# Kernel optimization log

Measured on AMD Instinct MI355X. Metric: run time of the kernel, lower is better.

The kernel has to match this reference:

```python
import jax, jax.numpy as jnp
import numpy as np

ALPHA = 1000.0  # softmin temperature from the original module


def setup_inputs() -> dict:
    key = jax.random.key(0)
    ks = jax.random.split(key, 10)
    B, D, H, E, K = 8192, 784, 256, 32, 512
    s = 0.05  # small init scale to keep activations/distances numerically sane
    return {
        "x": jax.random.normal(ks[0], (B, D), jnp.float32),
        "cluster_reps": jax.random.normal(ks[1], (K, E), jnp.float32),
        "W1": jax.random.normal(ks[2], (D, H), jnp.float32) * s,
        "b1": jnp.zeros((H,), jnp.float32),
        "W2": jax.random.normal(ks[3], (H, E), jnp.float32) * s,
        "b2": jnp.zeros((E,), jnp.float32),
        "W3": jax.random.normal(ks[4], (E, H), jnp.float32) * s,
        "b3": jnp.zeros((H,), jnp.float32),
        "W4": jax.random.normal(ks[5], (H, D), jnp.float32) * s,
        "b4": jnp.zeros((D,), jnp.float32),
    }


def reference(x, cluster_reps, W1, b1, W2, b2, W3, b3, W4, b4):
    # --- autoencoder: 2-layer MLP encoder / decoder ---
    h = jax.nn.relu(x @ W1 + b1)            # [B, H]
    embeddings = h @ W2 + b2                # [B, E]
    h2 = jax.nn.relu(embeddings @ W3 + b3)  # [B, H]
    reconstruction = h2 @ W4 + b4           # [B, D]

    # --- squared distances to cluster reps: [B, K] ---
    diff = embeddings[:, None, :] - cluster_reps[None, :, :]  # [B, K, E]
    distances = jnp.sum(diff * diff, axis=2)                  # [B, K]

    # --- stable softmin-weighted distances ---
    min_dist = jnp.min(distances, axis=1, keepdims=True)       # [B, 1]
    exponentials = jnp.exp(-ALPHA * (distances - min_dist))    # [B, K]
    sum_exponentials = jnp.sum(exponentials, axis=1, keepdims=True)
    weighted_dists = distances * (exponentials / sum_exponentials)

    return (weighted_dists, distances, reconstruction, embeddings)
```

## Files before the change

### kernel.cpp

```cpp
#include <hip/hip_runtime.h>
#include <cstddef>

#define NB 8192
#define ND 784
#define NH 256
#define NE 32
#define NK 512
#define ALPHA_F 1000.0f

typedef _Float16 h8 __attribute__((ext_vector_type(8)));
typedef float f32x4 __attribute__((ext_vector_type(4)));

#define TW1 25
#define TN1 8
#define NBW1 200
#define TW4 8
#define TN4 25
#define NBW4 200
#define NBW2 8
#define NBW3 8

__global__ __launch_bounds__(256)
void prep4_kernel(const float* __restrict__ W1, _Float16* __restrict__ w1thi,
                  _Float16* __restrict__ w1tlo,
                  const float* __restrict__ W4, _Float16* __restrict__ w4thi,
                  _Float16* __restrict__ w4tlo,
                  const float* __restrict__ W2, _Float16* __restrict__ w2thi,
                  _Float16* __restrict__ w2tlo,
                  const float* __restrict__ W3, _Float16* __restrict__ w3thi,
                  _Float16* __restrict__ w3tlo) {
    __shared__ float tile[32][33];
    const int b   = blockIdx.x;
    const int tid = threadIdx.x;

    const float* W; _Float16 *hi, *lo; int K, N, kt, nt;
    if (b < NBW1) {
        W = W1; hi = w1thi; lo = w1tlo; K = ND; N = NH;
        kt = b % TW1; nt = b / TW1;
    } else if (b < NBW1 + NBW4) {
        const int bb = b - NBW1;
        W = W4; hi = w4thi; lo = w4tlo; K = NH; N = ND;
        kt = bb % TW4; nt = bb / TW4;
    } else if (b < NBW1 + NBW4 + NBW2) {
        W = W2; hi = w2thi; lo = w2tlo; K = NH; N = NE;
        kt = b - (NBW1 + NBW4); nt = 0;
    } else {
        W = W3; hi = w3thi; lo = w3tlo; K = NE; N = NH;
        kt = 0; nt = b - (NBW1 + NBW4 + NBW2);
    }
    const int k0 = kt * 32, n0 = nt * 32;
    const int row = tid >> 3, c4 = (tid & 7) * 4;
    #pragma unroll
    for (int j = 0; j < 4; ++j) {
        const int k = k0 + row, n = n0 + c4 + j;
        tile[row][c4 + j] = (k < K && n < N) ? W[(size_t)k * N + n] : 0.f;
    }
    __syncthreads();
    const int n = n0 + row;
    if (n < N) {
        #pragma unroll
        for (int j = 0; j < 4; ++j) {
            const int k = k0 + c4 + j;
            if (k < K) {
                float w = tile[c4 + j][row];
                _Float16 hh = (_Float16)w;
                float r = w - (float)hh;
                hi[(size_t)n * K + k] = hh;
                lo[(size_t)n * K + k] = (_Float16)(r * 2048.0f);
            }
        }
    }
}

__global__ __launch_bounds__(512, 1)
void mega_kernel(const float* __restrict__ x, const float* __restrict__ reps,
                 const _Float16* __restrict__ w1thi, const _Float16* __restrict__ w1tlo,
                 const _Float16* __restrict__ w2thi, const _Float16* __restrict__ w2tlo,
                 const _Float16* __restrict__ w3thi, const _Float16* __restrict__ w3tlo,
                 const _Float16* __restrict__ w4thi, const _Float16* __restrict__ w4tlo,
                 const float* __restrict__ b1, const float* __restrict__ b2,
                 const float* __restrict__ b3, const float* __restrict__ b4,
                 float* __restrict__ emb_g, float* __restrict__ recon_g,
                 float* __restrict__ dist_g, float* __restrict__ wout_g) {
    __shared__ __align__(16) unsigned char lds[135936];
    _Float16* R0h  = (_Float16*)lds;
    _Float16* sA   = (_Float16*)(lds + 81920);
    _Float16* hP   = (_Float16*)(lds + 92160);
    float*    es   = (float*)(lds + 125952);
    _Float16* eP   = (_Float16*)(lds + 130560);
    float*    rmin = (float*)(lds + 135680);
    float*    rinv = (float*)(lds + 135808);

    const int tid  = threadIdx.x;
    const int lane = tid & 63;
    const int wv   = tid >> 6;
    const int li   = lane & 15;
    const int kq   = (lane >> 4) * 8;
    const int quad = lane >> 4;
    const int r0   = blockIdx.x * 32;

    const float c1 = 1.0f / 2048.0f;
    const float c2 = c1 * c1;

    {
        _Float16* sBhi = R0h;
        _Float16* sBlo = R0h + 2 * 256 * 40;
        _Float16* sAhi = sA;
        _Float16* sAlo = sA + 2 * 32 * 40;
        const int arow = (tid & 127) >> 2;
        const int ak   = (tid & 3) * 8;
        const int brow = tid >> 1;
        const int bk   = (tid & 1) * 16;
        const float*    pA  = x + (size_t)(r0 + arow) * ND;
        const _Float16* pBh = w1thi + (size_t)brow * ND;
        const _Float16* pBl = w1tlo + (size_t)brow * ND;

        float araw[8];
        h8 rb0, rb1, rb2, rb3;

        auto pf = [&](int s) {
            if (tid < 128) {
                const int k = s * 32 + ak;
                if (k + 8 <= ND) {
                    f32x4 v0 = *(const f32x4*)(pA + k);
                    f32x4 v1 = *(const f32x4*)(pA + k + 4);
                    #pragma unroll
                    for (int j = 0; j < 4; ++j) {
                        araw[j] = v0[j]; araw[4 + j] = v1[j];
                    }
                } else {
                    #pragma unroll
                    for (int j = 0; j < 8; ++j) araw[j] = 0.f;
                }
            }
            const int kb = s * 32 + bk;
            rb0 = (kb + 8  <= ND) ? *(const h8*)(pBh + kb)     : (h8){};
            rb1 = (kb + 16 <= ND) ? *(const h8*)(pBh + kb + 8) : (h8){};
            rb2 = (kb + 8  <= ND) ? *(const h8*)(pBl + kb)     : (h8){};
            rb3 = (kb + 16 <= ND) ? *(const h8*)(pBl + kb + 8) : (h8){};
        };
        auto cm = [&](int buf) {
            if (tid < 128) {
                h8 hi, lo;
                #pragma unroll
                for (int j = 0; j < 8; ++j) {
                    float v = araw[j];
                    _Float16 hh = (_Float16)v;
                    hi[j] = hh;
                    lo[j] = (_Float16)((v - (float)hh) * 2048.0f);
                }
                *(h8*)&sAhi[buf * 32 * 40 + arow * 40 + ak] = hi;
                *(h8*)&sAlo[buf * 32 * 40 + arow * 40 + ak] = lo;
            }
            *(h8*)&sBhi[buf * 256 * 40 + brow * 40 + bk]     = rb0;
            *(h8*)&sBhi[buf * 256 * 40 + brow * 40 + bk + 8] = rb1;
            *(h8*)&sBlo[buf * 256 * 40 + brow * 40 + bk]     = rb2;
            *(h8*)&sBlo[buf * 256 * 40 + brow * 40 + bk + 8] = rb3;
        };

        pf(0); cm(0); pf(1);
        __syncthreads();

        f32x4 a0[2][2] = {}, a1[2][2] = {}, a2[2][2] = {};
        for (int s = 0; s < 25; ++s) {
            const int buf = s & 1;
            h8 fah[2], fal[2], fbh[2], fbl[2];
            #pragma unroll
            for (int mt = 0; mt < 2; ++mt) {
                const int ao = buf * 32 * 40 + (mt * 16 + li) * 40 + kq;
                fah[mt] = *(const h8*)&sAhi[ao];
                fal[mt] = *(const h8*)&sAlo[ao];
            }
            #pragma unroll
            for (int nt = 0; nt < 2; ++nt) {
                const int bo = buf * 256 * 40 + (wv * 32 + nt * 16 + li) * 40 + kq;
                fbh[nt] = *(const h8*)&sBhi[bo];
                fbl[nt] = *(const h8*)&sBlo[bo];
            }
            #pragma unroll
            for (int mt = 0; mt < 2; ++mt)
                #pragma unroll
                for (int nt = 0; nt < 2; ++nt) {
                    a0[mt][nt] = __builtin_amdgcn_mfma_f32_16x16x32_f16(
                        fah[mt], fbh[nt], a0[mt][nt], 0, 0, 0);
                    a1[mt][nt] = __builtin_amdgcn_mfma_f32_16x16x32_f16(
                        fah[mt], fbl[nt], a1[mt][nt], 0, 0, 0);
                    a1[mt][nt] = __builtin_amdgcn_mfma_f32_16x16x32_f16(
                        fal[mt], fbh[nt], a1[mt][nt], 0, 0, 0);
                    a2[mt][nt] = __builtin_amdgcn_mfma_f32_16x16x32_f16(
                        fal[mt], fbl[nt], a2[mt][nt], 0, 0, 0);
                }
            if (s + 1 < 25) { cm((s + 1) & 1); if (s + 2 < 25) pf(s + 2); }
            __syncthreads();
        }
        _Float16* hhi = hP;
        _Float16* hlo = hP + 32 * 264;
        #pragma unroll
        for (int nt = 0; nt < 2; ++nt) {
            const int n = wv * 32 + nt * 16 + li;
            const float bv = b1[n];
            #pragma unroll
            for (int mt = 0; mt < 2; ++mt)
                #pragma unroll
                for (int r = 0; r < 4; ++r) {
                    const int m = mt * 16 + quad * 4 + r;
                    float v = a0[mt][nt][r] + c1 * a1[mt][nt][r]
                            + c2 * a2[mt][nt][r] + bv;
                    v = fmaxf(v, 0.f);
                    _Float16 hh = (_Float16)v;
                    hhi[m * 264 + n] = hh;
                    hlo[m * 264 + n] = (_Float16)((v - (float)hh) * 2048.0f);
                }
        }
    }
    __syncthreads();

    {
        _Float16* w2h = R0h;
        _Float16* w2l = R0h + 32 * 264;
        #pragma unroll
        for (int i = 0; i < 2; ++i) {
            const int cc  = tid + i * 512;
            const int row = cc >> 5, off = (cc & 31) * 8;
            *(h8*)&w2h[row * 264 + off] = *(const h8*)(w2thi + row * 256 + off);
            *(h8*)&w2l[row * 264 + off] = *(const h8*)(w2tlo + row * 256 + off);
        }
    }
    __syncthreads();
    if (wv < 4) {
        const int mt = wv >> 1, nt = wv & 1;
        _Float16* hhi = hP;
        _Float16* hlo = hP + 32 * 264;
        _Float16* w2h = R0h;
        _Float16* w2l = R0h + 32 * 264;
        f32x4 e0 = {}, e1 = {}, e2 = {};
        #pragma unroll
        for (int ks = 0; ks < 8; ++ks) {
            h8 ah = *(const h8*)&hhi[(mt * 16 + li) * 264 + ks * 32 + kq];
            h8 al = *(const h8*)&hlo[(mt * 16 + li) * 264 + ks * 32 + kq];
            h8 bh = *(const h8*)&w2h[(nt * 16 + li) * 264 + ks * 32 + kq];
            h8 bl = *(const h8*)&w2l[(nt * 16 + li) * 264 + ks * 32 + kq];
            e0 = __builtin_amdgcn_mfma_f32_16x16x32_f16(ah, bh, e0, 0, 0, 0);
            e1 = __builtin_amdgcn_mfma_f32_16x16x32_f16(ah, bl, e1, 0, 0, 0);
            e1 = __builtin_amdgcn_mfma_f32_16x16x32_f16(al, bh, e1, 0, 0, 0);
            e2 = __builtin_amdgcn_mfma_f32_16x16x32_f16(al, bl, e2, 0, 0, 0);
        }
        const int ccol = nt * 16 + li;
        const float bv = b2[ccol];
        _Float16* ehi = eP;
        _Float16* elo = eP + 32 * 40;
        #pragma unroll
        for (int r = 0; r < 4; ++r) {
            const int m = mt * 16 + quad * 4 + r;
            float v = e0[r] + c1 * e1[r] + c2 * e2[r] + bv;
            es[m * 36 + ccol] = v;
            _Float16 hh = (_Float16)v;
            ehi[m * 40 + ccol] = hh;
            elo[m * 40 + ccol] = (_Float16)((v - (float)hh) * 2048.0f);
            emb_g[(size_t)(r0 + m) * NE + ccol] = v;
        }
    }
    __syncthreads();

    {
        _Float16* w3h = R0h;
        _Float16* w3l = R0h + 256 * 40;
        #pragma unroll
        for (int i = 0; i < 2; ++i) {
            const int cc  = tid + i * 512;
            const int row = cc >> 2, off = (cc & 3) * 8;
            *(h8*)&w3h[row * 40 + off] = *(const h8*)(w3thi + row * 32 + off);
            *(h8*)&w3l[row * 40 + off] = *(const h8*)(w3tlo + row * 32 + off);
        }
    }
    __syncthreads();
    {
        const int n0 = wv * 32;
        _Float16* w3h  = R0h;
        _Float16* w3l  = R0h + 256 * 40;
        _Float16* ehi  = eP;
        _Float16* elo  = eP + 32 * 40;
        _Float16* h2hi = hP;
        _Float16* h2lo = hP + 32 * 264;
        h8 ah[2], al[2];
        #pragma unroll
        for (int mt = 0; mt < 2; ++mt) {
            ah[mt] = *(const h8*)&ehi[(mt * 16 + li) * 40 + kq];
            al[mt] = *(const h8*)&elo[(mt * 16 + li) * 40 + kq];
        }
        #pragma unroll
        for (int nt = 0; nt < 2; ++nt) {
            h8 bh = *(const h8*)&w3h[(n0 + nt * 16 + li) * 40 + kq];
            h8 bl = *(const h8*)&w3l[(n0 + nt * 16 + li) * 40 + kq];
            const int col = n0 + nt * 16 + li;
            const float bv = b3[col];
            #pragma unroll
            for (int mt = 0; mt < 2; ++mt) {
                f32x4 q0 = {}, q1 = {}, q2 = {};
                q0 = __builtin_amdgcn_mfma_f32_16x16x32_f16(ah[mt], bh, q0, 0, 0, 0);
                q1 = __builtin_amdgcn_mfma_f32_16x16x32_f16(ah[mt], bl, q1, 0, 0, 0);
                q1 = __builtin_amdgcn_mfma_f32_16x16x32_f16(al[mt], bh, q1, 0, 0, 0);
                q2 = __builtin_amdgcn_mfma_f32_16x16x32_f16(al[mt], bl, q2, 0, 0, 0);
                #pragma unroll
                for (int r = 0; r < 4; ++r) {
                    const int m = mt * 16 + quad * 4 + r;
                    float v = q0[r] + c1 * q1[r] + c2 * q2[r] + bv;
                    v = fmaxf(v, 0.f);
                    _Float16 hh = (_Float16)v;
                    h2hi[m * 264 + col] = hh;
                    h2lo[m * 264 + col] = (_Float16)((v - (float)hh) * 2048.0f);
                }
            }
        }
    }
    __syncthreads();

    {
        _Float16* sBhi = R0h;
        _Float16* sBlo = R0h + 2 * 128 * 40;
        _Float16* h2hi = hP;
        _Float16* h2lo = hP + 32 * 264;
        const int brow = tid >> 2;
        const int bk4  = (tid & 3) * 8;
        h8 rbh, rbl;
        auto pf = [&](int ss) {
            int rg = (ss >> 3) * 128 + brow;
            if (rg > ND - 1) rg = ND - 1;
            const int k = (ss & 7) * 32 + bk4;
            rbh = *(const h8*)(w4thi + (size_t)rg * NH + k);
            rbl = *(const h8*)(w4tlo + (size_t)rg * NH + k);
        };
        auto cm = [&](int ss) {
            const int buf = ss & 1;
            *(h8*)&sBhi[buf * 128 * 40 + brow * 40 + bk4] = rbh;
            *(h8*)&sBlo[buf * 128 * 40 + brow * 40 + bk4] = rbl;
        };
        pf(0); cm(0); pf(1);
        __syncthreads();

        f32x4 q0[2] = {}, q1[2] = {};
        for (int ss = 0; ss < 56; ++ss) {
            const int buf = ss & 1, ks = ss & 7;
            h8 fbh = *(const h8*)&sBhi[buf * 128 * 40 + (wv * 16 + li) * 40 + kq];
            h8 fbl = *(const h8*)&sBlo[buf * 128 * 40 + (wv * 16 + li) * 40 + kq];
            #pragma unroll
            for (int mt = 0; mt < 2; ++mt) {
                h8 ah = *(const h8*)&h2hi[(mt * 16 + li) * 264 + ks * 32 + kq];
                h8 al = *(const h8*)&h2lo[(mt * 16 + li) * 264 + ks * 32 + kq];
                q0[mt] = __builtin_amdgcn_mfma_f32_16x16x32_f16(ah, fbh, q0[mt], 0, 0, 0);
                q1[mt] = __builtin_amdgcn_mfma_f32_16x16x32_f16(ah, fbl, q1[mt], 0, 0, 0);
                q1[mt] = __builtin_amdgcn_mfma_f32_16x16x32_f16(al, fbh, q1[mt], 0, 0, 0);
            }
            if (ss + 1 < 56) { cm(ss + 1); if (ss + 2 < 56) pf(ss + 2); }
            __syncthreads();
            if (ks == 7) {
                const int n = (ss >> 3) * 128 + wv * 16 + li;
                if (n < ND) {
                    const float bv = b4[n];
                    #pragma unroll
                    for (int mt = 0; mt < 2; ++mt)
                        #pragma unroll
                        for (int r = 0; r < 4; ++r) {
                            const int m = mt * 16 + quad * 4 + r;
                            recon_g[(size_t)(r0 + m) * ND + n] =
                                q0[mt][r] + c1 * q1[mt][r] + bv;
                        }
                }
                #pragma unroll
                for (int mt = 0; mt < 2; ++mt) { q0[mt] = {}; q1[mt] = {}; }
            }
        }
    }
    __syncthreads();

    {
        float* tr = (float*)R0h;
        const float* rp = reps + (size_t)tid * NE;
        f32x4 rv[8];
        #pragma unroll
        for (int e4 = 0; e4 < 8; ++e4) rv[e4] = ((const f32x4*)rp)[e4];

        float d[32];
        #pragma unroll
        for (int r = 0; r < 32; ++r) {
            float a = 0.f;
            #pragma unroll
            for (int e4 = 0; e4 < 8; ++e4) {
                f32x4 ev = *(const f32x4*)&es[r * 36 + e4 * 4];
                #pragma unroll
                for (int j = 0; j < 4; ++j) {
                    float t = ev[j] - rv[e4][j];
                    a = fmaf(t, t, a);
                }
            }
            d[r] = a;
            tr[r * 520 + tid] = a;
        }
        __syncthreads();
        #pragma unroll
        for (int p = 0; p < 4; ++p) {
            const int rr = wv * 4 + p;
            f32x4 a = *(const f32x4*)&tr[rr * 520 + lane * 8];
            f32x4 b = *(const f32x4*)&tr[rr * 520 + lane * 8 + 4];
            float m = fminf(fminf(fminf(a[0], a[1]), fminf(a[2], a[3])),
                            fminf(fminf(b[0], b[1]), fminf(b[2], b[3])));
            #pragma unroll
            for (int off = 32; off > 0; off >>= 1)
                m = fminf(m, __shfl_xor(m, off, 64));
            if (lane == 0) rmin[rr] = m;
        }
        __syncthreads();
        float e[32];
        #pragma unroll
        for (int r = 0; r < 32; ++r) {
            e[r] = expf(-ALPHA_F * (d[r] - rmin[r]));
            tr[r * 520 + tid] = e[r];
        }
        __syncthreads();
        #pragma unroll
        for (int p = 0; p < 4; ++p) {
            const int rr = wv * 4 + p;
            f32x4 a = *(const f32x4*)&tr[rr * 520 + lane * 8];
            f32x4 b = *(const f32x4*)&tr[rr * 520 + lane * 8 + 4];
            float s = ((a[0] + a[1]) + (a[2] + a[3])) +
                      ((b[0] + b[1]) + (b[2] + b[3]));
            #pragma unroll
            for (int off = 32; off > 0; off >>= 1)
                s += __shfl_xor(s, off, 64);
            if (lane == 0) rinv[rr] = 1.0f / s;
        }
        __syncthreads();
        #pragma unroll
        for (int r = 0; r < 32; ++r) {
            const size_t row = (size_t)(r0 + r);
            dist_g[row * NK + tid] = d[r];
            wout_g[row * NK + tid] = d[r] * (e[r] * rinv[r]);
        }
    }
}

__global__ __launch_bounds__(256)
void splitw2_kernel(const float* __restrict__ W1, _Float16* __restrict__ w1thi,
                    _Float16* __restrict__ w1tlo,
                    const float* __restrict__ W4, _Float16* __restrict__ w4thi,
                    _Float16* __restrict__ w4tlo) {
    const int b = blockIdx.x;
    const float* W; _Float16 *hi, *lo; int K, N, n;
    if (b < NH) { W = W1; hi = w1thi; lo = w1tlo; K = ND; N = NH; n = b; }
    else        { W = W4; hi = w4thi; lo = w4tlo; K = NH; N = ND; n = b - NH; }
    for (int k = threadIdx.x; k < K; k += 256) {
        float w = W[(size_t)k * N + n];
        _Float16 hh = (_Float16)w;
        float r = w - (float)hh;
        hi[(size_t)n * K + k] = hh;
        lo[(size_t)n * K + k] = (_Float16)(r * 2048.0f);
    }
}

template<int TERMS, bool RELU, bool SPLITA, int MT>
__global__ __launch_bounds__(256)
void mfma_gemm3(const float* __restrict__ Af32,
                const _Float16* __restrict__ Ahi_g,
                const _Float16* __restrict__ Alo_g,
                const _Float16* __restrict__ WThi,
                const _Float16* __restrict__ WTlo,
                const float* __restrict__ bias, float* __restrict__ C,
                int N, int K, int KS) {
    constexpr int BM  = MT * 32;
    constexpr int ACH = BM / 64;
    constexpr int AS  = BM * 40;
    constexpr int BS  = 64 * 40;
    __shared__ __align__(16) _Float16 smem[2 * BM * 40 * 2 + 2 * 64 * 40 * 2];
    _Float16* sAhi = smem;
    _Float16* sAlo = sAhi + 2 * BM * 40;
    _Float16* sBhi = sAlo + 2 * BM * 40;
    _Float16* sBlo = sBhi + 2 * 64 * 40;

    const int tid = threadIdx.x;
    const int bm  = blockIdx.x * BM;
    const int bn  = blockIdx.y * 64;

    const int arow = (ACH == 1) ? (tid >> 2) : (tid >> 1);
    const int ak   = (ACH == 1) ? ((tid & 3) * 8) : ((tid & 1) * 16);
    const int brow = tid >> 2;
    const int bk   = (tid & 3) * 8;

    const float*    pA32 = SPLITA ? Af32 + (size_t)(bm + arow) * K : nullptr;
    const _Float16* pAhi = SPLITA ? nullptr : Ahi_g + (size_t)(bm + arow) * K;
    const _Float16* pAlo = SPLITA ? nullptr : Alo_g + (size_t)(bm + arow) * K;
    int brow_g = bn + brow; if (brow_g > N - 1) brow_g = N - 1;
    const _Float16* pBhi = WThi + (size_t)brow_g * K;
    const _Float16* pBlo = WTlo + (size_t)brow_g * K;

    float araw[ACH * 8];
    h8 rahi[ACH], ralo[ACH];
    h8 rbhi, rblo;

    auto prefetch = [&](int s) {
        #pragma unroll
        for (int c = 0; c < ACH; ++c) {
            const int k = s * 32 + ak + c * 8;
            if (SPLITA) {
                if (k + 8 <= K) {
                    f32x4 v0 = *(const f32x4*)(pA32 + k);
                    f32x4 v1 = *(const f32x4*)(pA32 + k + 4);
                    #pragma unroll
                    for (int j = 0; j < 4; ++j) {
                        araw[c * 8 + j]     = v0[j];
                        araw[c * 8 + 4 + j] = v1[j];
                    }
                } else {
                    #pragma unroll
                    for (int j = 0; j < 8; ++j) araw[c * 8 + j] = 0.f;
                }
            } else {
                rahi[c] = (k + 8 <= K) ? *(const h8*)(pAhi + k) : (h8){};
                ralo[c] = (k + 8 <= K) ? *(const h8*)(pAlo + k) : (h8){};
            }
        }
        const int kb = s * 32 + bk;
        rbhi = (kb + 8 <= K) ? *(const h8*)(pBhi + kb) : (h8){};
        rblo = (kb + 8 <= K) ? *(const h8*)(pBlo + kb) : (h8){};
    };

    auto commit = [&](int buf) {
        #pragma unroll
        for (int c = 0; c < ACH; ++c) {
            h8 hi, lo;
            if (SPLITA) {
                #pragma unroll
                for (int j = 0; j < 8; ++j) {
                    float v = araw[c * 8 + j];
                    _Float16 hh = (_Float16)v;
                    hi[j] = hh;
                    lo[j] = (_Float16)((v - (float)hh) * 2048.0f);
                }
            } else { hi = rahi[c]; lo = ralo[c]; }
            *(h8*)&sAhi[buf * AS + arow * 40 + ak + c * 8] = hi;
            *(h8*)&sAlo[buf * AS + arow * 40 + ak + c * 8] = lo;
        }
        *(h8*)&sBhi[buf * BS + brow * 40 + bk] = rbhi;
        *(h8*)&sBlo[buf * BS + brow * 40 + bk] = rblo;
    };

    prefetch(0);
    commit(0);
    prefetch(1);
    __syncthreads();

    const int lane = tid & 63;
    const int wv   = tid >> 6;
    const int wm   = (wv >> 1) * (MT * 16);
    const int wn   = (wv & 1) * 32;
    const int li   = lane & 15;
    const int kq   = (lane >> 4) * 8;

    f32x4 acc0[MT][2] = {};
    f32x4 acc1[MT][2] = {};
    f32x4 acc2[MT][2] = {};

    for (int s = 0; s < KS; ++s) {
        const int buf = s & 1;
        h8 fahi[MT], falo[MT], fbhi[2], fblo[2];
        #pragma unroll
        for (int mt = 0; mt < MT; ++mt) {
            const int ao = buf * AS + (wm + mt * 16 + li) * 40 + kq;
            fahi[mt] = *(const h8*)&sAhi[ao];
            falo[mt] = *(const h8*)&sAlo[ao];
        }
        #pragma unroll
        for (int nt = 0; nt < 2; ++nt) {
            const int bo = buf * BS + (wn + nt * 16 + li) * 40 + kq;
            fbhi[nt] = *(const h8*)&sBhi[bo];
            fblo[nt] = *(const h8*)&sBlo[bo];
        }
        #pragma unroll
        for (int mt = 0; mt < MT; ++mt)
            #pragma unroll
            for (int nt = 0; nt < 2; ++nt) {
                acc0[mt][nt] = __builtin_amdgcn_mfma_f32_16x16x32_f16(
                    fahi[mt], fbhi[nt], acc0[mt][nt], 0, 0, 0);
                acc1[mt][nt] = __builtin_amdgcn_mfma_f32_16x16x32_f16(
                    fahi[mt], fblo[nt], acc1[mt][nt], 0, 0, 0);
                acc1[mt][nt] = __builtin_amdgcn_mfma_f32_16x16x32_f16(
                    falo[mt], fbhi[nt], acc1[mt][nt], 0, 0, 0);
                if (TERMS == 4)
                    acc2[mt][nt] = __builtin_amdgcn_mfma_f32_16x16x32_f16(
                        falo[mt], fblo[nt], acc2[mt][nt], 0, 0, 0);
            }
        if (s + 1 < KS) {
            commit((s + 1) & 1);
            if (s + 2 < KS) prefetch(s + 2);
        }
        __syncthreads();
    }

    const float c1 = 1.0f / 2048.0f;
    const float c2 = c1 * c1;
    const int quad = lane >> 4;
    #pragma unroll
    for (int nt = 0; nt < 2; ++nt) {
        const int n = bn + wn + nt * 16 + li;
        if (n < N) {
            const float bv = bias[n];
            #pragma unroll
            for (int mt = 0; mt < MT; ++mt) {
                #pragma unroll
                for (int r = 0; r < 4; ++r) {
                    const int m = bm + wm + mt * 16 + quad * 4 + r;
                    float v = acc0[mt][nt][r] + c1 * acc1[mt][nt][r];
                    if (TERMS == 4) v += c2 * acc2[mt][nt][r];
                    v += bv;
                    if (RELU) v = fmaxf(v, 0.f);
                    C[(size_t)m * N + n] = v;
                }
            }
        }
    }
}

__global__ __launch_bounds__(256)
void mid_kernel(const float* __restrict__ h, const float* __restrict__ W2,
                const float* __restrict__ b2, const float* __restrict__ W3,
                const float* __restrict__ b3, float* __restrict__ emb,
                _Float16* __restrict__ h2hi, _Float16* __restrict__ h2lo) {
    __shared__ float es[16][32];
    const int tid = threadIdx.x;
    const int r0  = blockIdx.x * 16;

    #pragma unroll
    for (int half = 0; half < 2; ++half) {
        const int o   = tid + half * 256;
        const int row = o >> 5;
        const int col = o & 31;
        const float* hrow = h + (size_t)(r0 + row) * NH;
        float acc0 = 0.f, acc1 = 0.f;
        #pragma unroll 4
        for (int k = 0; k < NH; k += 4) {
            float4 hv = *(const float4*)(hrow + k);
            acc0 = fmaf(hv.x, W2[(k + 0) * NE + col], acc0);
            acc1 = fmaf(hv.y, W2[(k + 1) * NE + col], acc1);
            acc0 = fmaf(hv.z, W2[(k + 2) * NE + col], acc0);
            acc1 = fmaf(hv.w, W2[(k + 3) * NE + col], acc1);
        }
        float v = acc0 + acc1 + b2[col];
        es[row][col] = v;
        emb[(size_t)r0 * NE + o] = v;
    }
    __syncthreads();

    const int col = tid;
    float acc[16];
    #pragma unroll
    for (int r = 0; r < 16; ++r) acc[r] = 0.f;
    #pragma unroll
    for (int k = 0; k < NE; ++k) {
        float w = W3[k * NH + col];
        #pragma unroll
        for (int r = 0; r < 16; ++r) acc[r] = fmaf(es[r][k], w, acc[r]);
    }
    const float bb = b3[col];
    #pragma unroll
    for (int r = 0; r < 16; ++r) {
        float v = acc[r] + bb;
        v = v > 0.f ? v : 0.f;
        _Float16 hh = (_Float16)v;
        float rr = v - (float)hh;
        h2hi[(size_t)(r0 + r) * NH + col] = hh;
        h2lo[(size_t)(r0 + r) * NH + col] = (_Float16)(rr * 2048.0f);
    }
}

__global__ __launch_bounds__(512, 4)
void dist_kernel(const float* __restrict__ emb, const float* __restrict__ reps,
                 float* __restrict__ dist, float* __restrict__ wout) {
    __shared__ float es[8][32];
    __shared__ float tr[8][520];
    __shared__ float rmin[8];
    __shared__ float rinv[8];

    const int tid = threadIdx.x;
    const int r0  = blockIdx.x * 8;

    if (tid < 256) es[tid >> 5][tid & 31] = emb[(size_t)r0 * NE + tid];

    const float* rp = reps + (size_t)tid * NE;
    f32x4 rv[8];
    #pragma unroll
    for (int e4 = 0; e4 < 8; ++e4) rv[e4] = ((const f32x4*)rp)[e4];
    __syncthreads();

    float d[8];
    #pragma unroll
    for (int r = 0; r < 8; ++r) {
        float a = 0.f;
        #pragma unroll
        for (int e4 = 0; e4 < 8; ++e4) {
            f32x4 ev = *(const f32x4*)&es[r][e4 * 4];
            #pragma unroll
            for (int j = 0; j < 4; ++j) {
                float t = ev[j] - rv[e4][j];
                a = fmaf(t, t, a);
            }
        }
        d[r] = a;
    }

    const int lane = tid & 63;
    const int wv   = tid >> 6;

    #pragma unroll
    for (int r = 0; r < 8; ++r) tr[r][tid] = d[r];
    __syncthreads();
    {
        f32x4 a = *(const f32x4*)&tr[wv][lane * 8];
        f32x4 b = *(const f32x4*)&tr[wv][lane * 8 + 4];
        float m = fminf(fminf(fminf(a[0], a[1]), fminf(a[2], a[3])),
                        fminf(fminf(b[0], b[1]), fminf(b[2], b[3])));
        #pragma unroll
        for (int off = 32; off > 0; off >>= 1)
            m = fminf(m, __shfl_xor(m, off, 64));
        if (lane == 0) rmin[wv] = m;
    }
    __syncthreads();

    float e[8];
    #pragma unroll
    for (int r = 0; r < 8; ++r) {
        e[r] = expf(-ALPHA_F * (d[r] - rmin[r]));
        tr[r][tid] = e[r];
    }
    __syncthreads();
    {
        f32x4 a = *(const f32x4*)&tr[wv][lane * 8];
        f32x4 b = *(const f32x4*)&tr[wv][lane * 8 + 4];
        float s = ((a[0] + a[1]) + (a[2] + a[3])) +
                  ((b[0] + b[1]) + (b[2] + b[3]));
        #pragma unroll
        for (int off = 32; off > 0; off >>= 1)
            s += __shfl_xor(s, off, 64);
        if (lane == 0) rinv[wv] = 1.0f / s;
    }
    __syncthreads();

    #pragma unroll
    for (int r = 0; r < 8; ++r) {
        const size_t row = (size_t)(r0 + r);
        dist[row * NK + tid] = d[r];
        wout[row * NK + tid] = d[r] * (e[r] * rinv[r]);
    }
}

extern "C" void kernel_launch(void* const* d_in, const int* in_sizes, int n_in,
                              void* d_out, int out_size, void* d_ws, size_t ws_size,
                              hipStream_t stream) {
    const float* x    = (const float*)d_in[0];
    const float* reps = (const float*)d_in[1];
    const float* W1   = (const float*)d_in[2];
    const float* b1   = (const float*)d_in[3];
    const float* W2   = (const float*)d_in[4];
    const float* b2   = (const float*)d_in[5];
    const float* W3   = (const float*)d_in[6];
    const float* b3   = (const float*)d_in[7];
    const float* W4   = (const float*)d_in[8];
    const float* b4   = (const float*)d_in[9];

    float* out   = (float*)d_out;
    float* wout  = out;
    float* dist  = out + (size_t)NB * NK;
    float* recon = out + (size_t)2 * NB * NK;
    float* emb   = out + (size_t)2 * NB * NK + (size_t)NB * ND;

    const size_t nW14 = (size_t)ND * NH;
    const size_t nW23 = (size_t)NE * NH;
    const size_t wneed = (4 * nW14 + 4 * nW23) * sizeof(_Float16);

    if (d_ws != nullptr && ws_size >= wneed) {
        _Float16* w1thi = (_Float16*)d_ws;
        _Float16* w1tlo = w1thi + nW14;
        _Float16* w4thi = w1tlo + nW14;
        _Float16* w4tlo = w4thi + nW14;
        _Float16* w2thi = w4tlo + nW14;
        _Float16* w2tlo = w2thi + nW23;
        _Float16* w3thi = w2tlo + nW23;
        _Float16* w3tlo = w3thi + nW23;

        prep4_kernel<<<NBW1 + NBW4 + NBW2 + NBW3, 256, 0, stream>>>(
            W1, w1thi, w1tlo, W4, w4thi, w4tlo,
            W2, w2thi, w2tlo, W3, w3thi, w3tlo);

        mega_kernel<<<NB / 32, 512, 0, stream>>>(
            x, reps, w1thi, w1tlo, w2thi, w2tlo, w3thi, w3tlo, w4thi, w4tlo,
            b1, b2, b3, b4, emb, recon, dist, wout);
    } else {
        float* h = dist;
        _Float16* h2hi  = (_Float16*)(dist + (size_t)NB * NH);
        _Float16* h2lo  = h2hi + (size_t)NB * NH;
        _Float16* w1thi = (_Float16*)wout;
        _Float16* w1tlo = w1thi + (size_t)NH * ND;
        _Float16* w4thi = w1tlo + (size_t)NH * ND;
        _Float16* w4tlo = w4thi + (size_t)ND * NH;

        splitw2_kernel<<<NH + ND, 256, 0, stream>>>(W1, w1thi, w1tlo,
                                                    W4, w4thi, w4tlo);
        mfma_gemm3<4, true, true, 2><<<dim3(128, 4), 256, 0, stream>>>(
            x, nullptr, nullptr, w1thi, w1tlo, b1, h, NH, ND, 25);
        mid_kernel<<<NB / 16, 256, 0, stream>>>(h, W2, b2, W3, b3,
                                                emb, h2hi, h2lo);
        mfma_gemm3<3, false, false, 4><<<dim3(64, 13), 256, 0, stream>>>(
            nullptr, h2hi, h2lo, w4thi, w4tlo, b4, recon, ND, NH, 8);
        dist_kernel<<<NB / 8, 512, 0, stream>>>(emb, reps, dist, wout);
    }
}
```

Measured before the change: 166.1 us.

## Double mega_kernel block to 1024 threads and split per-wave tiles across 16 waves

The fused kernel now launches 1024 threads (16 waves) per 32-row block instead of 512. The GEMM1, GEMM3 and GEMM4 stages are retiled so each wave owns one 16-wide N tile (or one M/N tile pair). The distance/softmin stage splits the 32 rows into two 16-row halves, each with its own LDS scratch, and recomputes exp at write-out instead of holding it in registers. The aim is more latency hiding per CU, given that the large LDS footprint allows only one block per CU. In exchange, each wave reuses less data from each LDS fragment load and the register budget per thread is tighter, so spills are possible.

```diff
diff --git a/kernel.cpp b/kernel.cpp
--- a/kernel.cpp
+++ b/kernel.cpp
@@ -72,7 +72,9 @@
     }
 }
 
-__global__ __launch_bounds__(512, 1)
+#define HSTR 264
+
+__global__ __launch_bounds__(1024, 4)
 void mega_kernel(const float* __restrict__ x, const float* __restrict__ reps,
                  const _Float16* __restrict__ w1thi, const _Float16* __restrict__ w1tlo,
                  const _Float16* __restrict__ w2thi, const _Float16* __restrict__ w2tlo,
@@ -87,7 +89,8 @@
     _Float16* sA   = (_Float16*)(lds + 81920);
     _Float16* hP   = (_Float16*)(lds + 92160);
     float*    es   = (float*)(lds + 125952);
-    _Float16* eP   = (_Float16*)(lds + 130560);
+    _Float16* eh   = (_Float16*)(lds + 130560);
+    _Float16* el   = (_Float16*)(lds + 133120);
     float*    rmin = (float*)(lds + 135680);
     float*    rinv = (float*)(lds + 135808);
 
@@ -107,16 +110,18 @@
         _Float16* sBlo = R0h + 2 * 256 * 40;
         _Float16* sAhi = sA;
         _Float16* sAlo = sA + 2 * 32 * 40;
-        const int arow = (tid & 127) >> 2;
+        const int arow = (tid & 255) >> 3;
+        const int aro  = tid >> 2;
         const int ak   = (tid & 3) * 8;
-        const int brow = tid >> 1;
-        const int bk   = (tid & 1) * 16;
-        const float*    pA  = x + (size_t)(r0 + arow) * ND;
+        const int brow = tid >> 2;
+        const int bk   = (tid & 3) * 8;
+        (void)arow;
+        const float*    pA  = x + (size_t)(r0 + aro) * ND;
         const _Float16* pBh = w1thi + (size_t)brow * ND;
         const _Float16* pBl = w1tlo + (size_t)brow * ND;
 
         float araw[8];
-        h8 rb0, rb1, rb2, rb3;
+        h8 rbh, rbl;
 
         auto pf = [&](int s) {
             if (tid < 128) {
@@ -134,10 +139,8 @@
                 }
             }
             const int kb = s * 32 + bk;
-            rb0 = (kb + 8  <= ND) ? *(const h8*)(pBh + kb)     : (h8){};
-            rb1 = (kb + 16 <= ND) ? *(const h8*)(pBh + kb + 8) : (h8){};
-            rb2 = (kb + 8  <= ND) ? *(const h8*)(pBl + kb)     : (h8){};
-            rb3 = (kb + 16 <= ND) ? *(const h8*)(pBl + kb + 8) : (h8){};
+            rbh = (kb + 8 <= ND) ? *(const h8*)(pBh + kb) : (h8){};
+            rbl = (kb + 8 <= ND) ? *(const h8*)(pBl + kb) : (h8){};
         };
         auto cm = [&](int buf) {
             if (tid < 128) {
@@ -149,115 +152,95 @@
                     hi[j] = hh;
                     lo[j] = (_Float16)((v - (float)hh) * 2048.0f);
                 }
-                *(h8*)&sAhi[buf * 32 * 40 + arow * 40 + ak] = hi;
-                *(h8*)&sAlo[buf * 32 * 40 + arow * 40 + ak] = lo;
-            }
-            *(h8*)&sBhi[buf * 256 * 40 + brow * 40 + bk]     = rb0;
-            *(h8*)&sBhi[buf * 256 * 40 + brow * 40 + bk + 8] = rb1;
-            *(h8*)&sBlo[buf * 256 * 40 + brow * 40 + bk]     = rb2;
-            *(h8*)&sBlo[buf * 256 * 40 + brow * 40 + bk + 8] = rb3;
+                *(h8*)&sAhi[buf * 32 * 40 + aro * 40 + ak] = hi;
+                *(h8*)&sAlo[buf * 32 * 40 + aro * 40 + ak] = lo;
+            }
+            *(h8*)&sBhi[buf * 256 * 40 + brow * 40 + bk] = rbh;
+            *(h8*)&sBlo[buf * 256 * 40 + brow * 40 + bk] = rbl;
         };
 
         pf(0); cm(0); pf(1);
         __syncthreads();
 
-        f32x4 a0[2][2] = {}, a1[2][2] = {}, a2[2][2] = {};
+        f32x4 a0[2] = {}, a1[2] = {}, a2[2] = {};
         for (int s = 0; s < 25; ++s) {
             const int buf = s & 1;
-            h8 fah[2], fal[2], fbh[2], fbl[2];
+            h8 fah[2], fal[2];
             #pragma unroll
             for (int mt = 0; mt < 2; ++mt) {
                 const int ao = buf * 32 * 40 + (mt * 16 + li) * 40 + kq;
                 fah[mt] = *(const h8*)&sAhi[ao];
                 fal[mt] = *(const h8*)&sAlo[ao];
             }
-            #pragma unroll
-            for (int nt = 0; nt < 2; ++nt) {
-                const int bo = buf * 256 * 40 + (wv * 32 + nt * 16 + li) * 40 + kq;
-                fbh[nt] = *(const h8*)&sBhi[bo];
-                fbl[nt] = *(const h8*)&sBlo[bo];
-            }
-            #pragma unroll
-            for (int mt = 0; mt < 2; ++mt)
-                #pragma unroll
-                for (int nt = 0; nt < 2; ++nt) {
-                    a0[mt][nt] = __builtin_amdgcn_mfma_f32_16x16x32_f16(
-                        fah[mt], fbh[nt], a0[mt][nt], 0, 0, 0);
-                    a1[mt][nt] = __builtin_amdgcn_mfma_f32_16x16x32_f16(
-                        fah[mt], fbl[nt], a1[mt][nt], 0, 0, 0);
-                    a1[mt][nt] = __builtin_amdgcn_mfma_f32_16x16x32_f16(
-                        fal[mt], fbh[nt], a1[mt][nt], 0, 0, 0);
-                    a2[mt][nt] = __builtin_amdgcn_mfma_f32_16x16x32_f16(
-                        fal[mt], fbl[nt], a2[mt][nt], 0, 0, 0);
-                }
+            const int bo = buf * 256 * 40 + (wv * 16 + li) * 40 + kq;
+            h8 fbh = *(const h8*)&sBhi[bo];
+            h8 fbl = *(const h8*)&sBlo[bo];
+            #pragma unroll
+            for (int mt = 0; mt < 2; ++mt) {
+                a0[mt] = __builtin_amdgcn_mfma_f32_16x16x32_f16(fah[mt], fbh, a0[mt], 0, 0, 0);
+                a1[mt] = __builtin_amdgcn_mfma_f32_16x16x32_f16(fah[mt], fbl, a1[mt], 0, 0, 0);
+                a1[mt] = __builtin_amdgcn_mfma_f32_16x16x32_f16(fal[mt], fbh, a1[mt], 0, 0, 0);
+                a2[mt] = __builtin_amdgcn_mfma_f32_16x16x32_f16(fal[mt], fbl, a2[mt], 0, 0, 0);
+            }
             if (s + 1 < 25) { cm((s + 1) & 1); if (s + 2 < 25) pf(s + 2); }
             __syncthreads();
         }
         _Float16* hhi = hP;
-        _Float16* hlo = hP + 32 * 264;
-        #pragma unroll
-        for (int nt = 0; nt < 2; ++nt) {
-            const int n = wv * 32 + nt * 16 + li;
-            const float bv = b1[n];
-            #pragma unroll
-            for (int mt = 0; mt < 2; ++mt)
-                #pragma unroll
-                for (int r = 0; r < 4; ++r) {
-                    const int m = mt * 16 + quad * 4 + r;
-                    float v = a0[mt][nt][r] + c1 * a1[mt][nt][r]
-                            + c2 * a2[mt][nt][r] + bv;
-                    v = fmaxf(v, 0.f);
-                    _Float16 hh = (_Float16)v;
-                    hhi[m * 264 + n] = hh;
-                    hlo[m * 264 + n] = (_Float16)((v - (float)hh) * 2048.0f);
-                }
-        }
+        _Float16* hlo = hP + 32 * HSTR;
+        const int n = wv * 16 + li;
+        const float bv = b1[n];
+        #pragma unroll
+        for (int mt = 0; mt < 2; ++mt)
+            #pragma unroll
+            for (int r = 0; r < 4; ++r) {
+                const int m = mt * 16 + quad * 4 + r;
+                float v = a0[mt][r] + c1 * a1[mt][r] + c2 * a2[mt][r] + bv;
+                v = fmaxf(v, 0.f);
+                _Float16 t = (_Float16)v;
+                hhi[m * HSTR + n] = t;
+                hlo[m * HSTR + n] = (_Float16)((v - (float)t) * 2048.0f);
+            }
     }
     __syncthreads();
 
     {
         _Float16* w2h = R0h;
-        _Float16* w2l = R0h + 32 * 264;
-        #pragma unroll
-        for (int i = 0; i < 2; ++i) {
-            const int cc  = tid + i * 512;
-            const int row = cc >> 5, off = (cc & 31) * 8;
-            *(h8*)&w2h[row * 264 + off] = *(const h8*)(w2thi + row * 256 + off);
-            *(h8*)&w2l[row * 264 + off] = *(const h8*)(w2tlo + row * 256 + off);
-        }
+        _Float16* w2l = R0h + 32 * HSTR;
+        const int row = tid >> 5, off = (tid & 31) * 8;
+        *(h8*)&w2h[row * HSTR + off] = *(const h8*)(w2thi + row * 256 + off);
+        *(h8*)&w2l[row * HSTR + off] = *(const h8*)(w2tlo + row * 256 + off);
     }
     __syncthreads();
     if (wv < 4) {
         const int mt = wv >> 1, nt = wv & 1;
         _Float16* hhi = hP;
-        _Float16* hlo = hP + 32 * 264;
+        _Float16* hlo = hP + 32 * HSTR;
         _Float16* w2h = R0h;
-        _Float16* w2l = R0h + 32 * 264;
+        _Float16* w2l = R0h + 32 * HSTR;
         f32x4 e0 = {}, e1 = {}, e2 = {};
         #pragma unroll
         for (int ks = 0; ks < 8; ++ks) {
-            h8 ah = *(const h8*)&hhi[(mt * 16 + li) * 264 + ks * 32 + kq];
-            h8 al = *(const h8*)&hlo[(mt * 16 + li) * 264 + ks * 32 + kq];
-            h8 bh = *(const h8*)&w2h[(nt * 16 + li) * 264 + ks * 32 + kq];
-            h8 bl = *(const h8*)&w2l[(nt * 16 + li) * 264 + ks * 32 + kq];
+            const int k = ks * 32 + kq;
+            h8 ah = *(const h8*)&hhi[(mt * 16 + li) * HSTR + k];
+            h8 al = *(const h8*)&hlo[(mt * 16 + li) * HSTR + k];
+            h8 bh = *(const h8*)&w2h[(nt * 16 + li) * HSTR + k];
+            h8 bl = *(const h8*)&w2l[(nt * 16 + li) * HSTR + k];
             e0 = __builtin_amdgcn_mfma_f32_16x16x32_f16(ah, bh, e0, 0, 0, 0);
             e1 = __builtin_amdgcn_mfma_f32_16x16x32_f16(ah, bl, e1, 0, 0, 0);
             e1 = __builtin_amdgcn_mfma_f32_16x16x32_f16(al, bh, e1, 0, 0, 0);
             e2 = __builtin_amdgcn_mfma_f32_16x16x32_f16(al, bl, e2, 0, 0, 0);
         }
-        const int ccol = nt * 16 + li;
-        const float bv = b2[ccol];
-        _Float16* ehi = eP;
-        _Float16* elo = eP + 32 * 40;
+        const int col = nt * 16 + li;
+        const float bv = b2[col];
         #pragma unroll
         for (int r = 0; r < 4; ++r) {
             const int m = mt * 16 + quad * 4 + r;
             float v = e0[r] + c1 * e1[r] + c2 * e2[r] + bv;
-            es[m * 36 + ccol] = v;
-            _Float16 hh = (_Float16)v;
-            ehi[m * 40 + ccol] = hh;
-            elo[m * 40 + ccol] = (_Float16)((v - (float)hh) * 2048.0f);
-            emb_g[(size_t)(r0 + m) * NE + ccol] = v;
+            es[m * 36 + col] = v;
+            _Float16 t = (_Float16)v;
+            eh[m * 40 + col] = t;
+            el[m * 40 + col] = (_Float16)((v - (float)t) * 2048.0f);
+            emb_g[(size_t)(r0 + m) * NE + col] = v;
         }
     }
     __syncthreads();
@@ -265,51 +248,41 @@
     {
         _Float16* w3h = R0h;
         _Float16* w3l = R0h + 256 * 40;
-        #pragma unroll
-        for (int i = 0; i < 2; ++i) {
-            const int cc  = tid + i * 512;
-            const int row = cc >> 2, off = (cc & 3) * 8;
-            *(h8*)&w3h[row * 40 + off] = *(const h8*)(w3thi + row * 32 + off);
-            *(h8*)&w3l[row * 40 + off] = *(const h8*)(w3tlo + row * 32 + off);
-        }
+        const int row = tid >> 2, off = (tid & 3) * 8;
+        *(h8*)&w3h[row * 40 + off] = *(const h8*)(w3thi + row * 32 + off);
+        *(h8*)&w3l[row * 40 + off] = *(const h8*)(w3tlo + row * 32 + off);
     }
     __syncthreads();
     {
-        const int n0 = wv * 32;
         _Float16* w3h  = R0h;
         _Float16* w3l  = R0h + 256 * 40;
-        _Float16* ehi  = eP;
-        _Float16* elo  = eP + 32 * 40;
-        _Float16* h2hi = hP;
-        _Float16* h2lo = hP + 32 * 264;
+        _Float16* h2h  = hP;
+        _Float16* h2l  = hP + 32 * HSTR;
         h8 ah[2], al[2];
         #pragma unroll
         for (int mt = 0; mt < 2; ++mt) {
-            ah[mt] = *(const h8*)&ehi[(mt * 16 + li) * 40 + kq];
-            al[mt] = *(const h8*)&elo[(mt * 16 + li) * 40 + kq];
-        }
-        #pragma unroll
-        for (int nt = 0; nt < 2; ++nt) {
-            h8 bh = *(const h8*)&w3h[(n0 + nt * 16 + li) * 40 + kq];
-            h8 bl = *(const h8*)&w3l[(n0 + nt * 16 + li) * 40 + kq];
-            const int col = n0 + nt * 16 + li;
-            const float bv = b3[col];
-            #pragma unroll
-            for (int mt = 0; mt < 2; ++mt) {
-                f32x4 q0 = {}, q1 = {}, q2 = {};
-                q0 = __builtin_amdgcn_mfma_f32_16x16x32_f16(ah[mt], bh, q0, 0, 0, 0);
-                q1 = __builtin_amdgcn_mfma_f32_16x16x32_f16(ah[mt], bl, q1, 0, 0, 0);
-                q1 = __builtin_amdgcn_mfma_f32_16x16x32_f16(al[mt], bh, q1, 0, 0, 0);
-                q2 = __builtin_amdgcn_mfma_f32_16x16x32_f16(al[mt], bl, q2, 0, 0, 0);
-                #pragma unroll
-                for (int r = 0; r < 4; ++r) {
-                    const int m = mt * 16 + quad * 4 + r;
-                    float v = q0[r] + c1 * q1[r] + c2 * q2[r] + bv;
-                    v = fmaxf(v, 0.f);
-                    _Float16 hh = (_Float16)v;
-                    h2hi[m * 264 + col] = hh;
-                    h2lo[m * 264 + col] = (_Float16)((v - (float)hh) * 2048.0f);
-                }
+            ah[mt] = *(const h8*)&eh[(mt * 16 + li) * 40 + kq];
+            al[mt] = *(const h8*)&el[(mt * 16 + li) * 40 + kq];
+        }
+        const int col = wv * 16 + li;
+        h8 bh = *(const h8*)&w3h[col * 40 + kq];
+        h8 bl = *(const h8*)&w3l[col * 40 + kq];
+        const float bv = b3[col];
+        #pragma unroll
+        for (int mt = 0; mt < 2; ++mt) {
+            f32x4 q0 = {}, q1 = {}, q2 = {};
+            q0 = __builtin_amdgcn_mfma_f32_16x16x32_f16(ah[mt], bh, q0, 0, 0, 0);
+            q1 = __builtin_amdgcn_mfma_f32_16x16x32_f16(ah[mt], bl, q1, 0, 0, 0);
+            q1 = __builtin_amdgcn_mfma_f32_16x16x32_f16(al[mt], bh, q1, 0, 0, 0);
+            q2 = __builtin_amdgcn_mfma_f32_16x16x32_f16(al[mt], bl, q2, 0, 0, 0);
+            #pragma unroll
+            for (int r = 0; r < 4; ++r) {
+                const int m = mt * 16 + quad * 4 + r;
+                float v = q0[r] + c1 * q1[r] + c2 * q2[r] + bv;
+                v = fmaxf(v, 0.f);
+                _Float16 t = (_Float16)v;
+                h2h[m * HSTR + col] = t;
+                h2l[m * HSTR + col] = (_Float16)((v - (float)t) * 2048.0f);
             }
         }
     }
@@ -318,75 +291,82 @@
     {
         _Float16* sBhi = R0h;
         _Float16* sBlo = R0h + 2 * 128 * 40;
-        _Float16* h2hi = hP;
-        _Float16* h2lo = hP + 32 * 264;
+        _Float16* h2h  = hP;
+        _Float16* h2l  = hP + 32 * HSTR;
+        const int mt  = wv >> 3;
+        const int ntw = wv & 7;
         const int brow = tid >> 2;
         const int bk4  = (tid & 3) * 8;
         h8 rbh, rbl;
         auto pf = [&](int ss) {
-            int rg = (ss >> 3) * 128 + brow;
-            if (rg > ND - 1) rg = ND - 1;
-            const int k = (ss & 7) * 32 + bk4;
-            rbh = *(const h8*)(w4thi + (size_t)rg * NH + k);
-            rbl = *(const h8*)(w4tlo + (size_t)rg * NH + k);
+            if (tid < 512) {
+                int rg = (ss >> 3) * 128 + brow;
+                if (rg > ND - 1) rg = ND - 1;
+                const int k = (ss & 7) * 32 + bk4;
+                rbh = *(const h8*)(w4thi + (size_t)rg * NH + k);
+                rbl = *(const h8*)(w4tlo + (size_t)rg * NH + k);
+            }
         };
         auto cm = [&](int ss) {
-            const int buf = ss & 1;
-            *(h8*)&sBhi[buf * 128 * 40 + brow * 40 + bk4] = rbh;
-            *(h8*)&sBlo[buf * 128 * 40 + brow * 40 + bk4] = rbl;
+            if (tid < 512) {
+                const int buf = ss & 1;
+                *(h8*)&sBhi[buf * 128 * 40 + brow * 40 + bk4] = rbh;
+                *(h8*)&sBlo[buf * 128 * 40 + brow * 40 + bk4] = rbl;
+            }
         };
         pf(0); cm(0); pf(1);
         __syncthreads();
 
-        f32x4 q0[2] = {}, q1[2] = {};
+        f32x4 q0 = {}, q1 = {};
         for (int ss = 0; ss < 56; ++ss) {
             const int buf = ss & 1, ks = ss & 7;
-            h8 fbh = *(const h8*)&sBhi[buf * 128 * 40 + (wv * 16 + li) * 40 + kq];
-            h8 fbl = *(const h8*)&sBlo[buf * 128 * 40 + (wv * 16 + li) * 40 + kq];
-            #pragma unroll
-            for (int mt = 0; mt < 2; ++mt) {
-                h8 ah = *(const h8*)&h2hi[(mt * 16 + li) * 264 + ks * 32 + kq];
-                h8 al = *(const h8*)&h2lo[(mt * 16 + li) * 264 + ks * 32 + kq];
-                q0[mt] = __builtin_amdgcn_mfma_f32_16x16x32_f16(ah, fbh, q0[mt], 0, 0, 0);
-                q1[mt] = __builtin_amdgcn_mfma_f32_16x16x32_f16(ah, fbl, q1[mt], 0, 0, 0);
-                q1[mt] = __builtin_amdgcn_mfma_f32_16x16x32_f16(al, fbh, q1[mt], 0, 0, 0);
-            }
+            const int bo = buf * 128 * 40 + (ntw * 16 + li) * 40 + kq;
+            h8 fbh = *(const h8*)&sBhi[bo];
+            h8 fbl = *(const h8*)&sBlo[bo];
+            const int k = ks * 32 + kq;
+            h8 ah = *(const h8*)&h2h[(mt * 16 + li) * HSTR + k];
+            h8 al = *(const h8*)&h2l[(mt * 16 + li) * HSTR + k];
+            q0 = __builtin_amdgcn_mfma_f32_16x16x32_f16(ah, fbh, q0, 0, 0, 0);
+            q1 = __builtin_amdgcn_mfma_f32_16x16x32_f16(ah, fbl, q1, 0, 0, 0);
+            q1 = __builtin_amdgcn_mfma_f32_16x16x32_f16(al, fbh, q1, 0, 0, 0);
             if (ss + 1 < 56) { cm(ss + 1); if (ss + 2 < 56) pf(ss + 2); }
             __syncthreads();
             if (ks == 7) {
-                const int n = (ss >> 3) * 128 + wv * 16 + li;
+                const int n = (ss >> 3) * 128 + ntw * 16 + li;
                 if (n < ND) {
                     const float bv = b4[n];
                     #pragma unroll
-                    for (int mt = 0; mt < 2; ++mt)
-                        #pragma unroll
-                        for (int r = 0; r < 4; ++r) {
-                            const int m = mt * 16 + quad * 4 + r;
-                            recon_g[(size_t)(r0 + m) * ND + n] =
-                                q0[mt][r] + c1 * q1[mt][r] + bv;
-                        }
+                    for (int r = 0; r < 4; ++r) {
+                        const int m = mt * 16 + quad * 4 + r;
+                        recon_g[(size_t)(r0 + m) * ND + n] = q0[r] + c1 * q1[r] + bv;
+                    }
                 }
-                #pragma unroll
-                for (int mt = 0; mt < 2; ++mt) { q0[mt] = {}; q1[mt] = {}; }
+                q0 = {}; q1 = {};
             }
         }
     }
     __syncthreads();
 
     {
-        float* tr = (float*)R0h;
-        const float* rp = reps + (size_t)tid * NE;
+        float* tr0 = (float*)lds;
+        float* tr1 = (float*)(lds + 33280);
+        const int half = tid >> 9;
+        const int cl   = tid & 511;
+        float* trh = half ? tr1 : tr0;
+        const int rbase = half * 16;
+
+        const float* rp = reps + (size_t)cl * NE;
         f32x4 rv[8];
         #pragma unroll
         for (int e4 = 0; e4 < 8; ++e4) rv[e4] = ((const f32x4*)rp)[e4];
 
-        float d[32];
-        #pragma unroll
-        for (int r = 0; r < 32; ++r) {
+        float d[16];
+        #pragma unroll
+        for (int r = 0; r < 16; ++r) {
             float a = 0.f;
             #pragma unroll
             for (int e4 = 0; e4 < 8; ++e4) {
-                f32x4 ev = *(const f32x4*)&es[r * 36 + e4 * 4];
+                f32x4 ev = *(const f32x4*)&es[(rbase + r) * 36 + e4 * 4];
                 #pragma unroll
                 for (int j = 0; j < 4; ++j) {
                     float t = ev[j] - rv[e4][j];
@@ -394,47 +374,51 @@
                 }
             }
             d[r] = a;
-            tr[r * 520 + tid] = a;
+            trh[r * 520 + cl] = a;
         }
         __syncthreads();
-        #pragma unroll
-        for (int p = 0; p < 4; ++p) {
-            const int rr = wv * 4 + p;
-            f32x4 a = *(const f32x4*)&tr[rr * 520 + lane * 8];
-            f32x4 b = *(const f32x4*)&tr[rr * 520 + lane * 8 + 4];
-            float m = fminf(fminf(fminf(a[0], a[1]), fminf(a[2], a[3])),
-                            fminf(fminf(b[0], b[1]), fminf(b[2], b[3])));
-            #pragma unroll
-            for (int off = 32; off > 0; off >>= 1)
-                m = fminf(m, __shfl_xor(m, off, 64));
-            if (lane == 0) rmin[rr] = m;
+        {
+            const int w8 = wv & 7;
+            #pragma unroll
+            for (int p = 0; p < 2; ++p) {
+                const int rl = w8 * 2 + p;
+                float m = trh[rl * 520 + lane];
+                #pragma unroll
+                for (int j = 1; j < 8; ++j)
+                    m = fminf(m, trh[rl * 520 + lane + 64 * j]);
+                #pragma unroll
+                for (int off = 32; off > 0; off >>= 1)
+                    m = fminf(m, __shfl_xor(m, off, 64));
+                if (lane == 0) rmin[rbase + rl] = m;
+            }
         }
         __syncthreads();
-        float e[32];
-        #pragma unroll
-        for (int r = 0; r < 32; ++r) {
-            e[r] = expf(-ALPHA_F * (d[r] - rmin[r]));
-            tr[r * 520 + tid] = e[r];
-        }
+        #pragma unroll
+        for (int r = 0; r < 16; ++r)
+            trh[r * 520 + cl] = expf(-ALPHA_F * (d[r] - rmin[rbase + r]));
         __syncthreads();
-        #pragma unroll
-        for (int p = 0; p < 4; ++p) {
-            const int rr = wv * 4 + p;
-            f32x4 a = *(const f32x4*)&tr[rr * 520 + lane * 8];
-            f32x4 b = *(const f32x4*)&tr[rr * 520 + lane * 8 + 4];
-            float s = ((a[0] + a[1]) + (a[2] + a[3])) +
-                      ((b[0] + b[1]) + (b[2] + b[3]));
-            #pragma unroll
-            for (int off = 32; off > 0; off >>= 1)
-                s += __shfl_xor(s, off, 64);
-            if (lane == 0) rinv[rr] = 1.0f / s;
+        {
+            const int w8 = wv & 7;
+            #pragma unroll
+            for (int p = 0; p < 2; ++p) {
+                const int rl = w8 * 2 + p;
+                float s = trh[rl * 520 + lane];
+                #pragma unroll
+                for (int j = 1; j < 8; ++j)
+                    s += trh[rl * 520 + lane + 64 * j];
+                #pragma unroll
+                for (int off = 32; off > 0; off >>= 1)
+                    s += __shfl_xor(s, off, 64);
+                if (lane == 0) rinv[rbase + rl] = 1.0f / s;
+            }
         }
         __syncthreads();
         #pragma unroll
-        for (int r = 0; r < 32; ++r) {
-            const size_t row = (size_t)(r0 + r);
-            dist_g[row * NK + tid] = d[r];
-            wout_g[row * NK + tid] = d[r] * (e[r] * rinv[r]);
+        for (int r = 0; r < 16; ++r) {
+            const size_t row = (size_t)(r0 + rbase + r);
+            const float ev = expf(-ALPHA_F * (d[r] - rmin[rbase + r]));
+            dist_g[row * NK + cl] = d[r];
+            wout_g[row * NK + cl] = d[r] * (ev * rinv[rbase + r]);
         }
     }
 }
@@ -789,7 +773,7 @@
             W1, w1thi, w1tlo, W4, w4thi, w4tlo,
             W2, w2thi, w2tlo, W3, w3thi, w3tlo);
 
-        mega_kernel<<<NB / 32, 512, 0, stream>>>(
+        mega_kernel<<<NB / 32, 1024, 0, stream>>>(
             x, reps, w1thi, w1tlo, w2thi, w2tlo, w3thi, w3tlo, w4thi, w4tlo,
             b1, b2, b3, b4, emb, recon, dist, wout);
     } else {
```

New measurement: 160.9 us. -3.1%, faster.
